# Kernel tuning notes

Measured on AMD Instinct MI355X. Metric: run time of the kernel, lower is better.

Reference implementation:

```python
import jax, jax.numpy as jnp
import numpy as np

BATCH, IN, HID, NCLS = 4096, 2048, 8192, 1000

def setup_inputs() -> dict:
    key = jax.random.key(0)
    kx, kk, kg = jax.random.split(key, 3)
    x = jax.random.normal(kx, (BATCH, IN), dtype=jnp.float32)
    # torch nn.Linear weights: kohonen [HID, IN], grossberg [NCLS, HID], init U(-1, 1)
    Wk = jax.random.uniform(kk, (HID, IN), dtype=jnp.float32, minval=-1.0, maxval=1.0)
    Wg = jax.random.uniform(kg, (NCLS, HID), dtype=jnp.float32, minval=-1.0, maxval=1.0)
    return {"x": x, "Wk": Wk, "Wg": Wg}

def reference(x, Wk, Wg):
    # L2-normalize each row
    xn = x / jnp.linalg.norm(x, axis=1, keepdims=True)  # [B, IN]
    kohonen_out = jnp.einsum('bi,hi->bh', xn, Wk)        # [B, HID]
    idx = jnp.argmax(kohonen_out, axis=1)                # [B] winner units
    # one-hot @ Wg.T == gather columns of Wg for winning units
    out = jnp.take(Wg, idx, axis=1).T                    # [B, NCLS]
    return out
```

## Files before the change

### kernel.cpp

```cpp
#include <hip/hip_runtime.h>
#include <stdint.h>

typedef unsigned int u32;
typedef unsigned long long u64;
typedef unsigned short u16;
typedef short short8 __attribute__((ext_vector_type(8)));
typedef float floatx4 __attribute__((ext_vector_type(4)));

#define BATCH 4096
#define IN    2048
#define HID   8192
#define NCLS  1000

#define OFF_ROWKEY 0u
#define OFF_TOPK   32768u
#define OFF_XB     8421376u
#define OFF_WKB    25198592u
#define OFF_WGT    58753024u
#define TOTAL_FULL 91521024ull

__device__ __forceinline__ u32 f2bf(float f) {
    u32 u = __float_as_uint(f);
    return (u + 0x7FFFu + ((u >> 16) & 1u)) >> 16;
}
__device__ __forceinline__ u32 fkey(float f) {
    u32 u = __float_as_uint(f);
    return (u & 0x80000000u) ? ~u : (u | 0x80000000u);
}
__device__ __forceinline__ float unfkey(u32 k) {
    return __uint_as_float((k & 0x80000000u) ? (k ^ 0x80000000u) : ~k);
}

__global__ __launch_bounds__(256) void prep_kernel(
    const float* __restrict__ x, const float* __restrict__ Wk,
    u32* __restrict__ xb, u32* __restrict__ wkb)
{
    const int gid = blockIdx.x * 256 + threadIdx.x;
    const int NSEG_X = BATCH * IN / 8;
    const int NSEG_W = HID * IN / 8;
    const int stride = gridDim.x * 256;
    for (int s = gid; s < NSEG_X + NSEG_W; s += stride) {
        const float* src;
        u32* dst;
        if (s < NSEG_X) { src = x + (size_t)s * 8;            dst = xb  + (size_t)s * 4; }
        else { int t = s - NSEG_X; src = Wk + (size_t)t * 8;  dst = wkb + (size_t)t * 4; }
        float4 a = ((const float4*)src)[0];
        float4 b = ((const float4*)src)[1];
        uint4 o;
        o.x = f2bf(a.x) | (f2bf(a.y) << 16);
        o.y = f2bf(a.z) | (f2bf(a.w) << 16);
        o.z = f2bf(b.x) | (f2bf(b.y) << 16);
        o.w = f2bf(b.z) | (f2bf(b.w) << 16);
        ((uint4*)dst)[0] = o;
    }
}

__global__ __launch_bounds__(256) void transpose_wg_kernel(
    const float* __restrict__ Wg, float* __restrict__ WgT)
{
    __shared__ float t[32][33];
    const int bx = blockIdx.x * 32;
    const int by = blockIdx.y * 32;
    const int tx = threadIdx.x & 31, ty = threadIdx.x >> 5;
    #pragma unroll
    for (int i = 0; i < 32; i += 8) {
        int c = by + ty + i;
        t[ty + i][tx] = (c < NCLS) ? Wg[(size_t)c * HID + bx + tx] : 0.f;
    }
    __syncthreads();
    #pragma unroll
    for (int i = 0; i < 32; i += 8) {
        int c = by + tx;
        if (c < NCLS) WgT[(size_t)(bx + ty + i) * NCLS + by + tx] = t[tx][ty + i];
    }
}

__global__ __launch_bounds__(256) void mfma_gemm_kernel(
    const u16* __restrict__ xb, const u16* __restrict__ wkb,
    u64* __restrict__ topk)
{
    __shared__ u16 At[128 * 32];
    __shared__ u16 Bt[128 * 32];

    const int tid  = threadIdx.x;
    const int lane = tid & 63;
    const int w    = tid >> 6;
    const int bm   = blockIdx.y * 128;
    const int bn   = blockIdx.x * 128;
    const int wrow = (w >> 1) * 64, wcol = (w & 1) * 64;
    const int m = lane & 15, q = lane >> 4;

    floatx4 acc[4][4];
    #pragma unroll
    for (int i = 0; i < 4; i++)
        #pragma unroll
        for (int j = 0; j < 4; j++)
            acc[i][j] = (floatx4){0.f, 0.f, 0.f, 0.f};

    const int row0 = tid >> 2, k8_0 = tid & 3;
    const int row1 = (tid + 256) >> 2, k8_1 = (tid + 256) & 3;
    const u16* gxa0 = xb  + (size_t)(bm + row0) * IN + k8_0 * 8;
    const u16* gxa1 = xb  + (size_t)(bm + row1) * IN + k8_1 * 8;
    const u16* gwb0 = wkb + (size_t)(bn + row0) * IN + k8_0 * 8;
    const u16* gwb1 = wkb + (size_t)(bn + row1) * IN + k8_1 * 8;

    for (int k0 = 0; k0 < IN; k0 += 32) {
        __builtin_amdgcn_global_load_lds(
            (const __attribute__((address_space(1))) u32*)(gxa0 + k0),
            (__attribute__((address_space(3))) u32*)&At[tid * 8], 16, 0, 0);
        __builtin_amdgcn_global_load_lds(
            (const __attribute__((address_space(1))) u32*)(gxa1 + k0),
            (__attribute__((address_space(3))) u32*)&At[(tid + 256) * 8], 16, 0, 0);
        __builtin_amdgcn_global_load_lds(
            (const __attribute__((address_space(1))) u32*)(gwb0 + k0),
            (__attribute__((address_space(3))) u32*)&Bt[tid * 8], 16, 0, 0);
        __builtin_amdgcn_global_load_lds(
            (const __attribute__((address_space(1))) u32*)(gwb1 + k0),
            (__attribute__((address_space(3))) u32*)&Bt[(tid + 256) * 8], 16, 0, 0);

        __syncthreads();

        short8 af[4], bfr[4];
        #pragma unroll
        for (int i = 0; i < 4; i++) {
            af[i]  = *(const short8*)&At[(wrow + i * 16 + m) * 32 + q * 8];
            bfr[i] = *(const short8*)&Bt[(wcol + i * 16 + m) * 32 + q * 8];
        }
        #pragma unroll
        for (int i = 0; i < 4; i++)
            #pragma unroll
            for (int j = 0; j < 4; j++)
                acc[i][j] = __builtin_amdgcn_mfma_f32_16x16x32_bf16(
                    af[i], bfr[j], acc[i][j], 0, 0, 0);

        __syncthreads();
    }

    const int g = blockIdx.x * 2 + (wcol >> 6);
    #pragma unroll
    for (int i = 0; i < 4; i++) {
        #pragma unroll
        for (int r = 0; r < 4; r++) {
            const int grow = bm + wrow + i * 16 + q * 4 + r;
            u64 b = 0ull, s = 0ull;
            #pragma unroll
            for (int j = 0; j < 4; j++) {
                const int gcol = bn + wcol + j * 16 + m;
                u64 k = ((u64)fkey(acc[i][j][r]) << 32) |
                        (u64)(0x1FFFu - (u32)gcol);
                if (k > b) { s = b; b = k; } else if (k > s) { s = k; }
            }
            #pragma unroll
            for (int off = 1; off < 16; off <<= 1) {
                u64 ob = __shfl_xor(b, off, 64);
                u64 os = __shfl_xor(s, off, 64);
                u64 nb = (b > ob) ? b : ob;
                u64 ns = (b > ob) ? ((ob > s) ? ob : s) : ((b > os) ? b : os);
                b = nb; s = ns;
            }
            if (m == 0) {
                ulonglong2 v; v.x = b; v.y = s;
                *(ulonglong2*)&topk[(size_t)grow * 256 + g * 2] = v;
            }
        }
    }
}

__global__ __launch_bounds__(256) void scan_kernel(
    const u64* __restrict__ topk,
    const float* __restrict__ x, const float* __restrict__ Wk,
    const float* __restrict__ WgT, float* __restrict__ out)
{
    __shared__ u64 wmax[4];
    __shared__ int cnt;
    __shared__ u64 candk[64];
    __shared__ float wpart[4];
    __shared__ int wincol;
    const int row = blockIdx.x;
    const int tid = threadIdx.x;
    if (tid == 0) cnt = 0;

    u64 key = topk[(size_t)row * 256 + tid];
    u64 mx = key;
    #pragma unroll
    for (int off = 1; off < 64; off <<= 1) {
        u64 o = __shfl_xor(mx, off, 64);
        if (o > mx) mx = o;
    }
    if ((tid & 63) == 0) wmax[tid >> 6] = mx;
    __syncthreads();
    u64 gmax = wmax[0];
    #pragma unroll
    for (int i = 1; i < 4; i++) if (wmax[i] > gmax) gmax = wmax[i];

    const float thr = unfkey((u32)(gmax >> 32)) - 1.0f;
    const float myv = unfkey((u32)(key >> 32));
    if (myv >= thr) { int c = atomicAdd(&cnt, 1); if (c < 64) candk[c] = key; }
    __syncthreads();
    const int n = min(cnt, 64);

    int col;
    if (n == 1) {
        col = 0x1FFF - (int)(candk[0] & 0xFFFFu);
    } else {
        u64 best = 0ull;
        const float4* xr = (const float4*)(x + (size_t)row * IN);
        const float4 a0 = xr[tid * 2], a1 = xr[tid * 2 + 1];
        for (int c = 0; c < n; c++) {
            const int h = 0x1FFF - (int)(candk[c] & 0xFFFFu);
            const float4* wr = (const float4*)(Wk + (size_t)h * IN);
            float4 b0 = wr[tid * 2], b1 = wr[tid * 2 + 1];
            float p = a0.x * b0.x + a0.y * b0.y + a0.z * b0.z + a0.w * b0.w
                    + a1.x * b1.x + a1.y * b1.y + a1.z * b1.z + a1.w * b1.w;
            #pragma unroll
            for (int off = 1; off < 64; off <<= 1) p += __shfl_xor(p, off, 64);
            if ((tid & 63) == 0) wpart[tid >> 6] = p;
            __syncthreads();
            if (tid == 0) {
                float sv = wpart[0] + wpart[1] + wpart[2] + wpart[3];
                u64 k2 = ((u64)fkey(sv) << 32) | (u64)(0x1FFFu - (u32)h);
                if (k2 > best) best = k2;
            }
            __syncthreads();
        }
        if (tid == 0) wincol = 0x1FFF - (int)(best & 0xFFFFu);
        __syncthreads();
        col = wincol;
    }

    const float* src = WgT + (size_t)col * NCLS;
    for (int c = tid; c < NCLS; c += 256)
        out[(size_t)row * NCLS + c] = src[c];
}

__global__ void init_ws_kernel(u64* rowkey) {
    int i = blockIdx.x * blockDim.x + threadIdx.x;
    if (i < BATCH) rowkey[i] = 0ULL;
}

__global__ __launch_bounds__(256) void gemm_argmax_kernel(
    const float* __restrict__ x, const float* __restrict__ Wk,
    u64* __restrict__ rowkey)
{
    __shared__ __align__(16) float As[32 * 64];
    __shared__ __align__(16) float Bs[32 * 64];
    const int tid = threadIdx.x;
    const int bm = blockIdx.y * 64, bn = blockIdx.x * 64;
    const int tx = tid & 15, ty = tid >> 4;
    float acc[4][4];
    #pragma unroll
    for (int i = 0; i < 4; i++)
        #pragma unroll
        for (int j = 0; j < 4; j++) acc[i][j] = 0.f;
    const int r0 = tid >> 3, q0 = tid & 7;
    const int r1 = (tid + 256) >> 3, q1 = (tid + 256) & 7;
    const float* xA0 = &x[(size_t)(bm + r0) * IN + q0 * 4];
    const float* xA1 = &x[(size_t)(bm + r1) * IN + q1 * 4];
    const float* wB0 = &Wk[(size_t)(bn + r0) * IN + q0 * 4];
    const float* wB1 = &Wk[(size_t)(bn + r1) * IN + q1 * 4];
    for (int k0 = 0; k0 < IN; k0 += 32) {
        float4 a0 = *(const float4*)(xA0 + k0);
        float4 a1 = *(const float4*)(xA1 + k0);
        float4 b0 = *(const float4*)(wB0 + k0);
        float4 b1 = *(const float4*)(wB1 + k0);
        __syncthreads();
        As[(q0 * 4 + 0) * 64 + r0] = a0.x; As[(q0 * 4 + 1) * 64 + r0] = a0.y;
        As[(q0 * 4 + 2) * 64 + r0] = a0.z; As[(q0 * 4 + 3) * 64 + r0] = a0.w;
        As[(q1 * 4 + 0) * 64 + r1] = a1.x; As[(q1 * 4 + 1) * 64 + r1] = a1.y;
        As[(q1 * 4 + 2) * 64 + r1] = a1.z; As[(q1 * 4 + 3) * 64 + r1] = a1.w;
        Bs[(q0 * 4 + 0) * 64 + r0] = b0.x; Bs[(q0 * 4 + 1) * 64 + r0] = b0.y;
        Bs[(q0 * 4 + 2) * 64 + r0] = b0.z; Bs[(q0 * 4 + 3) * 64 + r0] = b0.w;
        Bs[(q1 * 4 + 0) * 64 + r1] = b1.x; Bs[(q1 * 4 + 1) * 64 + r1] = b1.y;
        Bs[(q1 * 4 + 2) * 64 + r1] = b1.z; Bs[(q1 * 4 + 3) * 64 + r1] = b1.w;
        __syncthreads();
        #pragma unroll
        for (int k = 0; k < 32; k++) {
            float4 av = *(const float4*)&As[k * 64 + ty * 4];
            float4 bv = *(const float4*)&Bs[k * 64 + tx * 4];
            acc[0][0] += av.x * bv.x; acc[0][1] += av.x * bv.y;
            acc[0][2] += av.x * bv.z; acc[0][3] += av.x * bv.w;
            acc[1][0] += av.y * bv.x; acc[1][1] += av.y * bv.y;
            acc[1][2] += av.y * bv.z; acc[1][3] += av.y * bv.w;
            acc[2][0] += av.z * bv.x; acc[2][1] += av.z * bv.y;
            acc[2][2] += av.z * bv.z; acc[2][3] += av.z * bv.w;
            acc[3][0] += av.w * bv.x; acc[3][1] += av.w * bv.y;
            acc[3][2] += av.w * bv.z; acc[3][3] += av.w * bv.w;
        }
    }
    #pragma unroll
    for (int i = 0; i < 4; i++) {
        const int row = bm + ty * 4 + i;
        u64 best = 0ULL;
        #pragma unroll
        for (int j = 0; j < 4; j++) {
            const int col = bn + tx * 4 + j;
            u64 p = ((u64)fkey(acc[i][j]) << 32) | (u64)(0x1FFFu - (unsigned)col);
            if (p > best) best = p;
        }
        #pragma unroll
        for (int off = 1; off < 16; off <<= 1) {
            u64 other = __shfl_xor(best, off, 64);
            if (other > best) best = other;
        }
        if (tx == 0) atomicMax(&rowkey[row], best);
    }
}

__global__ __launch_bounds__(256) void gather_kernel(
    const u64* __restrict__ rowkey, const float* __restrict__ Wg,
    float* __restrict__ out)
{
    const int b = blockIdx.y;
    const int c = blockIdx.x * 256 + threadIdx.x;
    if (c >= NCLS) return;
    const int col = 0x1FFF - (int)(rowkey[b] & 0xFFFFFFFFu);
    out[(size_t)b * NCLS + c] = Wg[(size_t)c * HID + col];
}

extern "C" void kernel_launch(void* const* d_in, const int* in_sizes, int n_in,
                              void* d_out, int out_size, void* d_ws, size_t ws_size,
                              hipStream_t stream) {
    const float* x  = (const float*)d_in[0];
    const float* Wk = (const float*)d_in[1];
    const float* Wg = (const float*)d_in[2];
    float* out = (float*)d_out;
    char* ws = (char*)d_ws;

    if (ws_size >= TOTAL_FULL) {
        u64* topk  = (u64*)(ws + OFF_TOPK);
        u32* xb    = (u32*)(ws + OFF_XB);
        u32* wkb   = (u32*)(ws + OFF_WKB);
        float* WgT = (float*)(ws + OFF_WGT);

        hipLaunchKernelGGL(prep_kernel, dim3(2048), dim3(256), 0, stream,
                           x, Wk, xb, wkb);
        hipLaunchKernelGGL(transpose_wg_kernel, dim3(256, 32), dim3(256), 0, stream,
                           Wg, WgT);
        hipLaunchKernelGGL(mfma_gemm_kernel, dim3(HID / 128, BATCH / 128), dim3(256), 0, stream,
                           (const u16*)xb, (const u16*)wkb, topk);
        hipLaunchKernelGGL(scan_kernel, dim3(BATCH), dim3(256), 0, stream,
                           topk, x, Wk, WgT, out);
    } else {
        u64* rowkey = (u64*)(ws + OFF_ROWKEY);
        hipLaunchKernelGGL(init_ws_kernel, dim3(16), dim3(256), 0, stream, rowkey);
        hipLaunchKernelGGL(gemm_argmax_kernel, dim3(HID / 64, BATCH / 64), dim3(256), 0, stream,
                           x, Wk, rowkey);
        hipLaunchKernelGGL(gather_kernel, dim3(4, BATCH), dim3(256), 0, stream,
                           rowkey, Wg, out);
    }
}
```

Before: 350.5 us.

## Switch screening GEMM to FP8 scaled MFMA with top-4 candidates and wider rescoring

```diff
diff --git a/kernel.cpp b/kernel.cpp
--- a/kernel.cpp
+++ b/kernel.cpp
@@ -4,7 +4,8 @@
 typedef unsigned int u32;
 typedef unsigned long long u64;
 typedef unsigned short u16;
-typedef short short8 __attribute__((ext_vector_type(8)));
+typedef unsigned char u8;
+typedef int intx8 __attribute__((ext_vector_type(8)));
 typedef float floatx4 __attribute__((ext_vector_type(4)));
 
 #define BATCH 4096
@@ -14,15 +15,11 @@
 
 #define OFF_ROWKEY 0u
 #define OFF_TOPK   32768u
-#define OFF_XB     8421376u
-#define OFF_WKB    25198592u
-#define OFF_WGT    58753024u
-#define TOTAL_FULL 91521024ull
-
-__device__ __forceinline__ u32 f2bf(float f) {
-    u32 u = __float_as_uint(f);
-    return (u + 0x7FFFu + ((u >> 16) & 1u)) >> 16;
-}
+#define OFF_X8     16809984u
+#define OFF_WK8    25198592u
+#define OFF_WGT    41975808u
+#define TOTAL_FULL 74743808ull
+
 __device__ __forceinline__ u32 fkey(float f) {
     u32 u = __float_as_uint(f);
     return (u & 0x80000000u) ? ~u : (u | 0x80000000u);
@@ -30,57 +27,69 @@
 __device__ __forceinline__ float unfkey(u32 k) {
     return __uint_as_float((k & 0x80000000u) ? (k ^ 0x80000000u) : ~k);
 }
+__device__ __forceinline__ void ce(u64& a, u64& b) {
+    u64 mx = a > b ? a : b;
+    u64 mn = a > b ? b : a;
+    a = mx; b = mn;
+}
 
 __global__ __launch_bounds__(256) void prep_kernel(
     const float* __restrict__ x, const float* __restrict__ Wk,
-    u32* __restrict__ xb, u32* __restrict__ wkb)
-{
-    const int gid = blockIdx.x * 256 + threadIdx.x;
-    const int NSEG_X = BATCH * IN / 8;
-    const int NSEG_W = HID * IN / 8;
-    const int stride = gridDim.x * 256;
-    for (int s = gid; s < NSEG_X + NSEG_W; s += stride) {
-        const float* src;
-        u32* dst;
-        if (s < NSEG_X) { src = x + (size_t)s * 8;            dst = xb  + (size_t)s * 4; }
-        else { int t = s - NSEG_X; src = Wk + (size_t)t * 8;  dst = wkb + (size_t)t * 4; }
-        float4 a = ((const float4*)src)[0];
-        float4 b = ((const float4*)src)[1];
-        uint4 o;
-        o.x = f2bf(a.x) | (f2bf(a.y) << 16);
-        o.y = f2bf(a.z) | (f2bf(a.w) << 16);
-        o.z = f2bf(b.x) | (f2bf(b.y) << 16);
-        o.w = f2bf(b.z) | (f2bf(b.w) << 16);
-        ((uint4*)dst)[0] = o;
-    }
-}
-
-__global__ __launch_bounds__(256) void transpose_wg_kernel(
-    const float* __restrict__ Wg, float* __restrict__ WgT)
+    const float* __restrict__ Wg,
+    u8* __restrict__ x8, u8* __restrict__ wk8, float* __restrict__ WgT)
 {
     __shared__ float t[32][33];
-    const int bx = blockIdx.x * 32;
-    const int by = blockIdx.y * 32;
-    const int tx = threadIdx.x & 31, ty = threadIdx.x >> 5;
-    #pragma unroll
-    for (int i = 0; i < 32; i += 8) {
-        int c = by + ty + i;
-        t[ty + i][tx] = (c < NCLS) ? Wg[(size_t)c * HID + bx + tx] : 0.f;
-    }
-    __syncthreads();
-    #pragma unroll
-    for (int i = 0; i < 32; i += 8) {
-        int c = by + tx;
-        if (c < NCLS) WgT[(size_t)(bx + ty + i) * NCLS + by + tx] = t[tx][ty + i];
-    }
-}
-
-__global__ __launch_bounds__(256) void mfma_gemm_kernel(
-    const u16* __restrict__ xb, const u16* __restrict__ wkb,
+    const int bid = blockIdx.x;
+    if (bid < 1024) {
+        const int gid = bid * 256 + threadIdx.x;
+        const int NSX = BATCH * IN / 16;
+        const int NS  = NSX + HID * IN / 16;
+        for (int s = gid; s < NS; s += 1024 * 256) {
+            const float4* src; u8* dst;
+            if (s < NSX) { src = (const float4*)x + (size_t)s * 4;  dst = x8  + (size_t)s * 16; }
+            else { int u = s - NSX; src = (const float4*)Wk + (size_t)u * 4; dst = wk8 + (size_t)u * 16; }
+            uint4 o;
+            float4 f;
+            int p;
+            f = src[0];
+            p = __builtin_amdgcn_cvt_pk_fp8_f32(f.x, f.y, 0, false);
+            p = __builtin_amdgcn_cvt_pk_fp8_f32(f.z, f.w, p, true);  o.x = (u32)p;
+            f = src[1];
+            p = __builtin_amdgcn_cvt_pk_fp8_f32(f.x, f.y, 0, false);
+            p = __builtin_amdgcn_cvt_pk_fp8_f32(f.z, f.w, p, true);  o.y = (u32)p;
+            f = src[2];
+            p = __builtin_amdgcn_cvt_pk_fp8_f32(f.x, f.y, 0, false);
+            p = __builtin_amdgcn_cvt_pk_fp8_f32(f.z, f.w, p, true);  o.z = (u32)p;
+            f = src[3];
+            p = __builtin_amdgcn_cvt_pk_fp8_f32(f.x, f.y, 0, false);
+            p = __builtin_amdgcn_cvt_pk_fp8_f32(f.z, f.w, p, true);  o.w = (u32)p;
+            *(uint4*)dst = o;
+        }
+    } else {
+        const int tb = bid - 1024;
+        const int bx = (tb & 255) * 32;
+        const int by = (tb >> 8) * 32;
+        const int tx = threadIdx.x & 31, ty = threadIdx.x >> 5;
+        #pragma unroll
+        for (int i = 0; i < 32; i += 8) {
+            int c = by + ty + i;
+            t[ty + i][tx] = (c < NCLS) ? Wg[(size_t)c * HID + bx + tx] : 0.f;
+        }
+        __syncthreads();
+        #pragma unroll
+        for (int i = 0; i < 32; i += 8) {
+            int c = by + tx;
+            if (c < NCLS) WgT[(size_t)(bx + ty + i) * NCLS + by + tx] = t[tx][ty + i];
+        }
+    }
+}
+
+__global__ __launch_bounds__(256) void mfma_fp8_gemm_kernel(
+    const u8* __restrict__ x8, const u8* __restrict__ wk8,
     u64* __restrict__ topk)
 {
-    __shared__ u16 At[128 * 32];
-    __shared__ u16 Bt[128 * 32];
+    __shared__ u8 At[128 * 128];
+    __shared__ u8 Bt[128 * 128];
 
     const int tid  = threadIdx.x;
     const int lane = tid & 63;
@@ -97,70 +106,90 @@
         for (int j = 0; j < 4; j++)
             acc[i][j] = (floatx4){0.f, 0.f, 0.f, 0.f};
 
-    const int row0 = tid >> 2, k8_0 = tid & 3;
-    const int row1 = (tid + 256) >> 2, k8_1 = (tid + 256) & 3;
-    const u16* gxa0 = xb  + (size_t)(bm + row0) * IN + k8_0 * 8;
-    const u16* gxa1 = xb  + (size_t)(bm + row1) * IN + k8_1 * 8;
-    const u16* gwb0 = wkb + (size_t)(bn + row0) * IN + k8_0 * 8;
-    const u16* gwb1 = wkb + (size_t)(bn + row1) * IN + k8_1 * 8;
-
-    for (int k0 = 0; k0 < IN; k0 += 32) {
-        __builtin_amdgcn_global_load_lds(
-            (const __attribute__((address_space(1))) u32*)(gxa0 + k0),
-            (__attribute__((address_space(3))) u32*)&At[tid * 8], 16, 0, 0);
-        __builtin_amdgcn_global_load_lds(
-            (const __attribute__((address_space(1))) u32*)(gxa1 + k0),
-            (__attribute__((address_space(3))) u32*)&At[(tid + 256) * 8], 16, 0, 0);
-        __builtin_amdgcn_global_load_lds(
-            (const __attribute__((address_space(1))) u32*)(gwb0 + k0),
-            (__attribute__((address_space(3))) u32*)&Bt[tid * 8], 16, 0, 0);
-        __builtin_amdgcn_global_load_lds(
-            (const __attribute__((address_space(1))) u32*)(gwb1 + k0),
-            (__attribute__((address_space(3))) u32*)&Bt[(tid + 256) * 8], 16, 0, 0);
-
-        __syncthreads();
-
-        short8 af[4], bfr[4];
+    const int srow = tid >> 3;
+    const int soff = ((tid & 7) ^ (srow & 7)) * 16;
+    const u8* gA[4];
+    const u8* gB[4];
+    #pragma unroll
+    for (int s = 0; s < 4; s++) {
+        gA[s] = x8  + (size_t)(bm + s * 32 + srow) * IN + soff;
+        gB[s] = wk8 + (size_t)(bn + s * 32 + srow) * IN + soff;
+    }
+    const int fo1 = ((2 * q)     ^ (m & 7)) * 16;
+    const int fo2 = ((2 * q + 1) ^ (m & 7)) * 16;
+
+    for (int k0 = 0; k0 < IN; k0 += 128) {
+        #pragma unroll
+        for (int s = 0; s < 4; s++) {
+            __builtin_amdgcn_global_load_lds(
+                (const __attribute__((address_space(1))) u32*)(gA[s] + k0),
+                (__attribute__((address_space(3))) u32*)&At[s * 4096 + tid * 16], 16, 0, 0);
+            __builtin_amdgcn_global_load_lds(
+                (const __attribute__((address_space(1))) u32*)(gB[s] + k0),
+                (__attribute__((address_space(3))) u32*)&Bt[s * 4096 + tid * 16], 16, 0, 0);
+        }
+        __syncthreads();
+
+        intx8 af[4], bf[4];
         #pragma unroll
         for (int i = 0; i < 4; i++) {
-            af[i]  = *(const short8*)&At[(wrow + i * 16 + m) * 32 + q * 8];
-            bfr[i] = *(const short8*)&Bt[(wcol + i * 16 + m) * 32 + q * 8];
+            const int ra = (wrow + i * 16 + m) * 128;
+            int4 lo = *(const int4*)&At[ra + fo1];
+            int4 hi = *(const int4*)&At[ra + fo2];
+            af[i] = (intx8){lo.x, lo.y, lo.z, lo.w, hi.x, hi.y, hi.z, hi.w};
+            const int rb = (wcol + i * 16 + m) * 128;
+            int4 lo2 = *(const int4*)&Bt[rb + fo1];
+            int4 hi2 = *(const int4*)&Bt[rb + fo2];
+            bf[i] = (intx8){lo2.x, lo2.y, lo2.z, lo2.w, hi2.x, hi2.y, hi2.z, hi2.w};
         }
         #pragma unroll
         for (int i = 0; i < 4; i++)
             #pragma unroll
             for (int j = 0; j < 4; j++)
-                acc[i][j] = __builtin_amdgcn_mfma_f32_16x16x32_bf16(
-                    af[i], bfr[j], acc[i][j], 0, 0, 0);
-
-        __syncthreads();
-    }
-
-    const int g = blockIdx.x * 2 + (wcol >> 6);
+                acc[i][j] = __builtin_amdgcn_mfma_scale_f32_16x16x128_f8f6f4(
+                    af[i], bf[j], acc[i][j],
+                    0, 0,
+                    0, 0x7F,
+                    0, 0x7F);
+
+        __syncthreads();
+    }
+
+    const int g4 = (blockIdx.x * 2 + (wcol >> 6)) * 4;
     #pragma unroll
     for (int i = 0; i < 4; i++) {
         #pragma unroll
         for (int r = 0; r < 4; r++) {
-            const int grow = bm + wrow + i * 16 + q * 4 + r;
-            u64 b = 0ull, s = 0ull;
-            #pragma unroll
-            for (int j = 0; j < 4; j++) {
-                const int gcol = bn + wcol + j * 16 + m;
-                u64 k = ((u64)fkey(acc[i][j][r]) << 32) |
-                        (u64)(0x1FFFu - (u32)gcol);
-                if (k > b) { s = b; b = k; } else if (k > s) { s = k; }
-            }
+            u64 k0, k1, k2, k3;
+            {
+                const int c0 = bn + wcol + 0 * 16 + m;
+                const int c1 = bn + wcol + 1 * 16 + m;
+                const int c2 = bn + wcol + 2 * 16 + m;
+                const int c3 = bn + wcol + 3 * 16 + m;
+                k0 = ((u64)fkey(acc[i][0][r]) << 32) | (u64)(0x1FFFu - (u32)c0);
+                k1 = ((u64)fkey(acc[i][1][r]) << 32) | (u64)(0x1FFFu - (u32)c1);
+                k2 = ((u64)fkey(acc[i][2][r]) << 32) | (u64)(0x1FFFu - (u32)c2);
+                k3 = ((u64)fkey(acc[i][3][r]) << 32) | (u64)(0x1FFFu - (u32)c3);
+            }
+            ce(k0, k1); ce(k2, k3); ce(k0, k2); ce(k1, k3); ce(k1, k2);
             #pragma unroll
             for (int off = 1; off < 16; off <<= 1) {
-                u64 ob = __shfl_xor(b, off, 64);
-                u64 os = __shfl_xor(s, off, 64);
-                u64 nb = (b > ob) ? b : ob;
-                u64 ns = (b > ob) ? ((ob > s) ? ob : s) : ((b > os) ? b : os);
-                b = nb; s = ns;
+                u64 b0 = __shfl_xor(k0, off, 64);
+                u64 b1 = __shfl_xor(k1, off, 64);
+                u64 b2 = __shfl_xor(k2, off, 64);
+                u64 b3 = __shfl_xor(k3, off, 64);
+                k0 = k0 > b3 ? k0 : b3;
+                k1 = k1 > b2 ? k1 : b2;
+                k2 = k2 > b1 ? k2 : b1;
+                k3 = k3 > b0 ? k3 : b0;
+                ce(k0, k2); ce(k1, k3); ce(k0, k1); ce(k2, k3);
             }
             if (m == 0) {
-                ulonglong2 v; v.x = b; v.y = s;
-                *(ulonglong2*)&topk[(size_t)grow * 256 + g * 2] = v;
+                const int grow = bm + wrow + i * 16 + q * 4 + r;
+                ulonglong2 v01; v01.x = k0; v01.y = k1;
+                ulonglong2 v23; v23.x = k2; v23.y = k3;
+                *(ulonglong2*)&topk[(size_t)grow * 512 + g4]     = v01;
+                *(ulonglong2*)&topk[(size_t)grow * 512 + g4 + 2] = v23;
             }
         }
     }
@@ -173,59 +202,57 @@
 {
     __shared__ u64 wmax[4];
     __shared__ int cnt;
-    __shared__ u64 candk[64];
-    __shared__ float wpart[4];
-    __shared__ int wincol;
-    const int row = blockIdx.x;
-    const int tid = threadIdx.x;
-    if (tid == 0) cnt = 0;
-
-    u64 key = topk[(size_t)row * 256 + tid];
-    u64 mx = key;
+    __shared__ u64 candk[128];
+    __shared__ u64 bestk;
+    const int row  = blockIdx.x;
+    const int tid  = threadIdx.x;
+    const int lane = tid & 63;
+    const int w    = tid >> 6;
+    if (tid == 0) { cnt = 0; bestk = 0ull; }
+
+    ulonglong2 kk = *(const ulonglong2*)&topk[(size_t)row * 512 + tid * 2];
+    u64 mx = kk.x > kk.y ? kk.x : kk.y;
     #pragma unroll
     for (int off = 1; off < 64; off <<= 1) {
         u64 o = __shfl_xor(mx, off, 64);
         if (o > mx) mx = o;
     }
-    if ((tid & 63) == 0) wmax[tid >> 6] = mx;
+    if (lane == 0) wmax[w] = mx;
     __syncthreads();
     u64 gmax = wmax[0];
     #pragma unroll
     for (int i = 1; i < 4; i++) if (wmax[i] > gmax) gmax = wmax[i];
 
-    const float thr = unfkey((u32)(gmax >> 32)) - 1.0f;
-    const float myv = unfkey((u32)(key >> 32));
-    if (myv >= thr) { int c = atomicAdd(&cnt, 1); if (c < 64) candk[c] = key; }
+    const float thr = unfkey((u32)(gmax >> 32)) - 12.0f;
+    if (unfkey((u32)(kk.x >> 32)) >= thr) { int c = atomicAdd(&cnt, 1); if (c < 128) candk[c] = kk.x; }
+    if (unfkey((u32)(kk.y >> 32)) >= thr) { int c = atomicAdd(&cnt, 1); if (c < 128) candk[c] = kk.y; }
     __syncthreads();
-    const int n = min(cnt, 64);
+    const int n = min(cnt, 128);
 
     int col;
-    if (n == 1) {
-        col = 0x1FFF - (int)(candk[0] & 0xFFFFu);
+    if (n <= 1) {
+        col = 0x1FFF - (int)(gmax & 0xFFFFu);
     } else {
-        u64 best = 0ull;
         const float4* xr = (const float4*)(x + (size_t)row * IN);
-        const float4 a0 = xr[tid * 2], a1 = xr[tid * 2 + 1];
-        for (int c = 0; c < n; c++) {
+        for (int c = w; c < n; c += 4) {
             const int h = 0x1FFF - (int)(candk[c] & 0xFFFFu);
             const float4* wr = (const float4*)(Wk + (size_t)h * IN);
-            float4 b0 = wr[tid * 2], b1 = wr[tid * 2 + 1];
-            float p = a0.x * b0.x + a0.y * b0.y + a0.z * b0.z + a0.w * b0.w
-                    + a1.x * b1.x + a1.y * b1.y + a1.z * b1.z + a1.w * b1.w;
+            float p = 0.f;
+            #pragma unroll
+            for (int pass = 0; pass < 8; pass++) {
+                float4 a = xr[pass * 64 + lane];
+                float4 b = wr[pass * 64 + lane];
+                p += a.x * b.x + a.y * b.y + a.z * b.z + a.w * b.w;
+            }
             #pragma unroll
             for (int off = 1; off < 64; off <<= 1) p += __shfl_xor(p, off, 64);
-            if ((tid & 63) == 0) wpart[tid >> 6] = p;
-            __syncthreads();
-            if (tid == 0) {
-                float sv = wpart[0] + wpart[1] + wpart[2] + wpart[3];
-                u64 k2 = ((u64)fkey(sv) << 32) | (u64)(0x1FFFu - (u32)h);
-                if (k2 > best) best = k2;
-            }
-            __syncthreads();
-        }
-        if (tid == 0) wincol = 0x1FFF - (int)(best & 0xFFFFu);
-        __syncthreads();
-        col = wincol;
+            if (lane == 0) {
+                u64 key = ((u64)fkey(p) << 32) | (u64)(0x1FFFu - (u32)h);
+                atomicMax(&bestk, key);
+            }
+        }
+        __syncthreads();
+        col = 0x1FFF - (int)(bestk & 0xFFFFu);
     }
 
     const float* src = WgT + (size_t)col * NCLS;
@@ -328,16 +355,14 @@
 
     if (ws_size >= TOTAL_FULL) {
         u64* topk  = (u64*)(ws + OFF_TOPK);
-        u32* xb    = (u32*)(ws + OFF_XB);
-        u32* wkb   = (u32*)(ws + OFF_WKB);
+        u8*  x8    = (u8*)(ws + OFF_X8);
+        u8*  wk8   = (u8*)(ws + OFF_WK8);
         float* WgT = (float*)(ws + OFF_WGT);
 
-        hipLaunchKernelGGL(prep_kernel, dim3(2048), dim3(256), 0, stream,
-                           x, Wk, xb, wkb);
-        hipLaunchKernelGGL(transpose_wg_kernel, dim3(256, 32), dim3(256), 0, stream,
-                           Wg, WgT);
-        hipLaunchKernelGGL(mfma_gemm_kernel, dim3(HID / 128, BATCH / 128), dim3(256), 0, stream,
-                           (const u16*)xb, (const u16*)wkb, topk);
+        hipLaunchKernelGGL(prep_kernel, dim3(1024 + 8192), dim3(256), 0, stream,
+                           x, Wk, Wg, x8, wk8, WgT);
+        hipLaunchKernelGGL(mfma_fp8_gemm_kernel, dim3(HID / 128, BATCH / 128), dim3(256), 0, stream,
+                           x8, wk8, topk);
         hipLaunchKernelGGL(scan_kernel, dim3(BATCH), dim3(256), 0, stream,
                            topk, x, Wk, WgT, out);
     } else {
```

After: 464.4 us. 32.5% more time.
